# Kernel optimization log

Measured on AMD Instinct MI355X. Metric: run time of the kernel, lower is better.

Reference implementation:

```python
import jax, jax.numpy as jnp
import numpy as np

K = 5
BN_EPS = 1e-5


def _knn(xyz1, xyz2, embedding_lens):
    # squared pairwise distances [B, N, S]
    d2 = (jnp.sum(xyz1 ** 2, -1)[:, :, None]
          + jnp.sum(xyz2 ** 2, -1)[:, None, :]
          - 2.0 * jnp.einsum('bnc,bsc->bns', xyz1, xyz2))
    S = xyz2.shape[1]
    valid2 = jnp.arange(S)[None, :] < embedding_lens[:, None]  # [B, S]
    d2 = jnp.where(valid2[:, None, :], d2, jnp.float32(1e10))
    neg, idx = jax.lax.top_k(-d2, K)  # K smallest distances
    return -neg, idx  # squared dists [B,N,K], indices [B,N,K]


def _masked_bn(x, mask_f, gamma, beta):
    # x: [B, N, C]; mask_f: [B, N, 1] float; stats over valid positions only
    cnt = jnp.sum(mask_f)
    mean = jnp.sum(x * mask_f, axis=(0, 1)) / cnt
    var = jnp.sum(((x - mean) ** 2) * mask_f, axis=(0, 1)) / cnt
    return (x - mean) * jax.lax.rsqrt(var + BN_EPS) * gamma + beta


def setup_inputs() -> dict:
    key = jax.random.key(0)
    ks = jax.random.split(key, 8)
    B, N, S, D1, D2 = 16, 2048, 512, 384, 384
    xyz1 = jax.random.normal(ks[0], (B, N, 3), jnp.float32)
    xyz2 = jax.random.normal(ks[1], (B, S, 3), jnp.float32)
    points1 = jax.random.normal(ks[2], (B, N, D1), jnp.float32)
    points2 = jax.random.normal(ks[3], (B, S, D2), jnp.float32)
    point_lens = jax.random.randint(ks[4], (B,), N // 2, N + 1).astype(jnp.int32)
    embedding_lens = jax.random.randint(ks[5], (B,), S // 2, S + 1).astype(jnp.int32)
    point_mask = jnp.arange(N)[None, :] < point_lens[:, None]  # [B, N] bool
    Cin = D1 + D2
    W0 = jax.random.normal(ks[6], (768, Cin), jnp.float32) * (1.0 / np.sqrt(Cin))
    W1 = jax.random.normal(ks[7], (384, 768), jnp.float32) * (1.0 / np.sqrt(768))
    return dict(xyz1=xyz1, xyz2=xyz2, points1=points1, points2=points2,
                point_lens=point_lens, embedding_lens=embedding_lens,
                point_mask=point_mask,
                W0=W0, g0=jnp.ones((768,), jnp.float32), b0=jnp.zeros((768,), jnp.float32),
                W1=W1, g1=jnp.ones((384,), jnp.float32), b1=jnp.zeros((384,), jnp.float32))


def reference(xyz1, xyz2, points1, points2, point_lens, embedding_lens,
              point_mask, W0, g0, b0, W1, g1, b1):
    B, N, _ = xyz1.shape
    D2 = points2.shape[-1]
    dists, idx = _knn(xyz1[..., :3], xyz2, embedding_lens)
    eps = jnp.finfo(dists.dtype).eps
    dist_recip = 1.0 / (dists + eps)                    # [B, N, K]
    weight = dist_recip / jnp.sum(dist_recip, axis=2, keepdims=True)
    # masked gather: points2[b, idx[b,n,k], :] -> [B, N, K, D2]
    gathered = jnp.take_along_axis(points2, idx.reshape(B, N * K)[..., None],
                                   axis=1).reshape(B, N, K, D2)
    interp = jnp.sum(gathered * weight[..., None], axis=2)  # [B, N, D2]
    x = jnp.concatenate([points1, interp], axis=-1)          # [B, N, D1+D2]
    mask_f = point_mask.astype(x.dtype)[..., None]           # [B, N, 1]
    for W, g, b in ((W0, g0, b0), (W1, g1, b1)):
        x = jnp.einsum('bnc,dc->bnd', x, W)  # 1x1 conv, no bias
        x = jax.nn.relu(_masked_bn(x, mask_f, g, b))
    return x
```

## Files before the change

kernel.cpp:

```cpp
#include <hip/hip_runtime.h>
#include <cstdint>
#include <cstddef>

typedef unsigned short u16;
typedef __bf16 bf16x8 __attribute__((ext_vector_type(8)));
typedef float    f32x4 __attribute__((ext_vector_type(4)));
typedef unsigned int u32x4 __attribute__((ext_vector_type(4)));
typedef unsigned short u16x4 __attribute__((ext_vector_type(4)));

constexpr int BB   = 16;
constexpr int NN   = 2048;
constexpr int SS   = 512;
constexpr int DD   = 384;
constexpr int CIN  = 768;
constexpr int HID  = 768;
constexpr int OUTC = 384;
constexpr int MROWS = BB * NN;
constexpr float KNN_EPS = 1.1920929e-07f;
constexpr float BN_EPS  = 1e-5f;

constexpr size_t OFF_W0B  = 0;
constexpr size_t OFF_W1B  = OFF_W0B  + (size_t)HID*CIN*2;
constexpr size_t OFF_IDX  = OFF_W1B  + (size_t)OUTC*HID*2;
constexpr size_t OFF_WGT  = OFF_IDX  + (size_t)MROWS*5*4;
constexpr size_t OFF_SUM1 = OFF_WGT  + (size_t)MROWS*5*4;
constexpr size_t OFF_SUM2 = OFF_SUM1 + (size_t)HID*2*4;
constexpr size_t OFF_COEF1= OFF_SUM2 + (size_t)OUTC*2*4;
constexpr size_t OFF_COEF2= OFF_COEF1+ (size_t)HID*2*4;
constexpr size_t OFF_XCAT = OFF_COEF2+ (size_t)OUTC*2*4;
constexpr size_t OFF_H1   = OFF_XCAT + (size_t)MROWS*CIN*2;

__device__ inline float bf2f(u16 u){ unsigned int i = ((unsigned int)u)<<16; float f; __builtin_memcpy(&f,&i,4); return f; }
__device__ inline u16 f2bf(float f){ unsigned int x; __builtin_memcpy(&x,&f,4);
  unsigned int r = (x + 0x7fffu + ((x>>16)&1u)) >> 16; return (u16)r; }

__device__ inline void async16(const void* g, void* l){
  __builtin_amdgcn_global_load_lds((const __attribute__((address_space(1))) void*)g,
                                   (__attribute__((address_space(3))) void*)l, 16, 0, 0);
}

__global__ void cvtw_kernel(const float* __restrict__ W0, const float* __restrict__ W1,
                            u16* __restrict__ W0b, u16* __restrict__ W1b){
  int t = blockIdx.x*256 + threadIdx.x;
  if (t < HID*CIN)  W0b[t] = f2bf(W0[t]);
  if (t < OUTC*HID) W1b[t] = f2bf(W1[t]);
}

__global__ __launch_bounds__(256) void knn_kernel(const float* __restrict__ xyz1,
                                                  const float* __restrict__ xyz2,
                                                  const int* __restrict__ elens,
                                                  int* __restrict__ idxO, float* __restrict__ wO){
  __shared__ f32x4 sp[SS];
  const int tid = threadIdx.x;
  const int wv = tid >> 6, lane = tid & 63;
  const int wg = blockIdx.x*4 + wv;
  const int b = wg >> 11;
  const int n = wg & (NN-1);
  for (int s = tid; s < SS; s += 256){
    float x = xyz2[((size_t)b*SS + s)*3 + 0];
    float y = xyz2[((size_t)b*SS + s)*3 + 1];
    float z = xyz2[((size_t)b*SS + s)*3 + 2];
    f32x4 v; v[0]=x; v[1]=y; v[2]=z; v[3]=x*x+y*y+z*z;
    sp[s]=v;
  }
  __syncthreads();
  const size_t qoff = ((size_t)b*NN + n)*3;
  const float qx = xyz1[qoff+0], qy = xyz1[qoff+1], qz = xyz1[qoff+2];
  const float qq = qx*qx + qy*qy + qz*qz;
  const int Sl = elens[b];

  float d0=1e30f,d1=1e30f,d2v=1e30f,d3=1e30f,d4=1e30f;
  int   i0=0,i1=0,i2=0,i3=0,i4=0;
  #pragma unroll
  for (int j=0;j<8;j++){
    const int s = lane + j*64;
    f32x4 v = sp[s];
    float d = (s < Sl) ? (qq + v[3] - 2.f*(qx*v[0] + qy*v[1] + qz*v[2])) : 1e30f;
    bool lt4=d<d4, lt3=d<d3, lt2=d<d2v, lt1=d<d1, lt0=d<d0;
    float nd4 = lt3 ? d3 : (lt4 ? d : d4); int ni4 = lt3 ? i3 : (lt4 ? s : i4);
    float nd3 = lt2 ? d2v: (lt3 ? d : d3); int ni3 = lt2 ? i2 : (lt3 ? s : i3);
    float nd2 = lt1 ? d1 : (lt2 ? d : d2v);int ni2 = lt1 ? i1 : (lt2 ? s : i2);
    float nd1 = lt0 ? d0 : (lt1 ? d : d1); int ni1 = lt0 ? i0 : (lt1 ? s : i1);
    float nd0 = lt0 ? d  : d0;             int ni0 = lt0 ? s  : i0;
    d4=nd4;i4=ni4; d3=nd3;i3=ni3; d2v=nd2;i2=ni2; d1=nd1;i1=ni1; d0=nd0;i0=ni0;
  }
  float outd[5]; int outi[5];
  #pragma unroll
  for (int r=0;r<5;r++){
    float bd = d0; int bs = i0;
    #pragma unroll
    for (int m=1;m<64;m<<=1){
      float od = __shfl_xor(bd, m, 64);
      int   os = __shfl_xor(bs, m, 64);
      if (od < bd || (od == bd && os < bs)){ bd = od; bs = os; }
    }
    outd[r]=bd; outi[r]=bs;
    if (d0 == bd && i0 == bs){ d0=d1;i0=i1; d1=d2v;i1=i2; d2v=d3;i2=i3; d3=d4;i3=i4; d4=1e30f;i4=0; }
  }
  if (lane == 0){
    float r0=1.f/(outd[0]+KNN_EPS), r1=1.f/(outd[1]+KNN_EPS), r2=1.f/(outd[2]+KNN_EPS),
          r3=1.f/(outd[3]+KNN_EPS), r4=1.f/(outd[4]+KNN_EPS);
    float inv = 1.f/(r0+r1+r2+r3+r4);
    size_t base = (size_t)wg*5;
    idxO[base+0]=outi[0]; idxO[base+1]=outi[1]; idxO[base+2]=outi[2]; idxO[base+3]=outi[3]; idxO[base+4]=outi[4];
    wO[base+0]=r0*inv; wO[base+1]=r1*inv; wO[base+2]=r2*inv; wO[base+3]=r3*inv; wO[base+4]=r4*inv;
  }
}

__global__ __launch_bounds__(384) void xcat_kernel(const float* __restrict__ p1,
                                                   const float* __restrict__ p2,
                                                   const int* __restrict__ idx,
                                                   const float* __restrict__ wgt,
                                                   u16* __restrict__ xcat){
  const int t = threadIdx.x;
  const int rloc = t / 96, c4 = t % 96;
  const int row = blockIdx.x*4 + rloc;
  const int b = row >> 11;
  const int c = c4*4;
  f32x4 v1 = *reinterpret_cast<const f32x4*>(p1 + (size_t)row*DD + c);
  size_t ib = (size_t)row*5;
  f32x4 acc = {0.f,0.f,0.f,0.f};
  #pragma unroll
  for (int k=0;k<5;k++){
    int id = idx[ib+k]; float w = wgt[ib+k];
    f32x4 g = *reinterpret_cast<const f32x4*>(p2 + ((size_t)b*SS + id)*DD + c);
    #pragma unroll
    for (int j=0;j<4;j++) acc[j] += w * g[j];
  }
  u16x4 o1, o2;
  #pragma unroll
  for (int j=0;j<4;j++){ o1[j] = f2bf(v1[j]); o2[j] = f2bf(acc[j]); }
  *reinterpret_cast<u16x4*>(xcat + (size_t)row*CIN + c)      = o1;
  *reinterpret_cast<u16x4*>(xcat + (size_t)row*CIN + DD + c) = o2;
}

__global__ __launch_bounds__(512, 6) void gemm1_kernel(const u16* __restrict__ A,
                                                       const u16* __restrict__ Bw,
                                                       u16* __restrict__ Cout,
                                                       const int* __restrict__ plen,
                                                       float* __restrict__ sums){
  constexpr int K   = CIN;
  constexpr int NC  = HID;
  constexpr int GX  = NC/128;
  constexpr int NT  = K/32;
  constexpr int NWG = GX*256;
  constexpr int CPX = NWG/8;
  __shared__ u16 Ash[2][128*32];
  __shared__ u16 Bsh[2][128*32];
  const int tid  = threadIdx.x;
  const int lane = tid & 63, wv = tid >> 6;
  const int wr = wv >> 2, wc = wv & 3;
  const int l15 = lane & 15, l16 = lane >> 4;
  const int swz = (l15 >> 1) & 3;

  const int logical = (blockIdx.x & 7)*CPX + (blockIdx.x >> 3);
  const int bn = logical % GX, bm = logical / GX;

  const int srow = tid >> 2;
  const int sk4  = (tid & 3) ^ ((tid >> 3) & 3);
  const u16* gA = A  + (size_t)(bm*128 + srow)*K + sk4*8;
  const u16* gB = Bw + (size_t)(bn*128 + srow)*K + sk4*8;
  const int dst = (wv*64)*16;

  auto stageA = [&](int tt, int bi){ async16(gA + tt*32, (char*)&Ash[bi][0] + dst); };
  auto stageB = [&](int tt, int bi){ async16(gB + tt*32, (char*)&Bsh[bi][0] + dst); };

  int aoff[4], boff[2];
  #pragma unroll
  for (int m=0;m<4;m++) aoff[m] = (wr*64 + m*16 + l15)*32 + ((l16 ^ swz) << 3);
  #pragma unroll
  for (int n=0;n<2;n++) boff[n] = (wc*32 + n*16 + l15)*32 + ((l16 ^ swz) << 3);

  f32x4 acc[4][2] = {};

  stageA(0,0); stageB(0,0); stageA(1,1); stageB(1,1);
  asm volatile("s_waitcnt vmcnt(2)" ::: "memory");
  __builtin_amdgcn_s_barrier();
  __builtin_amdgcn_sched_barrier(0);

  for (int t=0; t<NT; ++t){
    const int cur = t & 1;
    const int tt = (t+2 < NT) ? (t+2) : (NT-1);
    bf16x8 af0 = *reinterpret_cast<const bf16x8*>(&Ash[cur][aoff[0]]);
    bf16x8 af1 = *reinterpret_cast<const bf16x8*>(&Ash[cur][aoff[1]]);
    bf16x8 af2 = *reinterpret_cast<const bf16x8*>(&Ash[cur][aoff[2]]);
    bf16x8 af3 = *reinterpret_cast<const bf16x8*>(&Ash[cur][aoff[3]]);
    bf16x8 bv0 = *reinterpret_cast<const bf16x8*>(&Bsh[cur][boff[0]]);
    asm volatile("s_waitcnt lgkmcnt(0)" ::: "memory");
    __builtin_amdgcn_s_barrier();
    __builtin_amdgcn_sched_barrier(0);
    stageA(tt, cur);
    __builtin_amdgcn_s_setprio(1);
    acc[0][0] = __builtin_amdgcn_mfma_f32_16x16x32_bf16(af0, bv0, acc[0][0], 0,0,0);
    acc[1][0] = __builtin_amdgcn_mfma_f32_16x16x32_bf16(af1, bv0, acc[1][0], 0,0,0);
    acc[2][0] = __builtin_amdgcn_mfma_f32_16x16x32_bf16(af2, bv0, acc[2][0], 0,0,0);
    acc[3][0] = __builtin_amdgcn_mfma_f32_16x16x32_bf16(af3, bv0, acc[3][0], 0,0,0);
    __builtin_amdgcn_s_setprio(0);
    bf16x8 bv1 = *reinterpret_cast<const bf16x8*>(&Bsh[cur][boff[1]]);
    asm volatile("s_waitcnt lgkmcnt(0)" ::: "memory");
    __builtin_amdgcn_s_barrier();
    __builtin_amdgcn_sched_barrier(0);
    stageB(tt, cur);
    __builtin_amdgcn_s_setprio(1);
    acc[0][1] = __builtin_amdgcn_mfma_f32_16x16x32_bf16(af0, bv1, acc[0][1], 0,0,0);
    acc[1][1] = __builtin_amdgcn_mfma_f32_16x16x32_bf16(af1, bv1, acc[1][1], 0,0,0);
    acc[2][1] = __builtin_amdgcn_mfma_f32_16x16x32_bf16(af2, bv1, acc[2][1], 0,0,0);
    acc[3][1] = __builtin_amdgcn_mfma_f32_16x16x32_bf16(af3, bv1, acc[3][1], 0,0,0);
    __builtin_amdgcn_s_setprio(0);
    asm volatile("s_waitcnt vmcnt(2)" ::: "memory");
    __builtin_amdgcn_s_barrier();
    __builtin_amdgcn_sched_barrier(0);
  }
  asm volatile("s_waitcnt vmcnt(0)" ::: "memory");
  __syncthreads();

  #pragma unroll
  for (int m=0;m<4;m++){
    int r0 = bm*128 + wr*64 + m*16 + l16*4;
    #pragma unroll
    for (int n=0;n<2;n++){
      int c = bn*128 + wc*32 + n*16 + l15;
      #pragma unroll
      for (int r=0;r<4;r++)
        Cout[(size_t)(r0+r)*NC + c] = f2bf(acc[m][n][r]);
    }
  }

  const int pl = plen[bm >> 4];
  const int rbase = (bm & 15)*128 + wr*64 + l16*4;
  float cs[2] = {0.f,0.f}, cs2[2] = {0.f,0.f};
  #pragma unroll
  for (int m=0;m<4;m++){
    #pragma unroll
    for (int r=0;r<4;r++){
      if (rbase + m*16 + r < pl){
        #pragma unroll
        for (int n=0;n<2;n++){
          float v = acc[m][n][r];
          cs[n] += v; cs2[n] += v*v;
        }
      }
    }
  }
  #pragma unroll
  for (int n=0;n<2;n++){
    cs[n]  += __shfl_xor(cs[n], 16, 64);  cs[n]  += __shfl_xor(cs[n], 32, 64);
    cs2[n] += __shfl_xor(cs2[n], 16, 64); cs2[n] += __shfl_xor(cs2[n], 32, 64);
  }
  float* lsum = (float*)&Ash[0][0];
  if (tid < 256) lsum[tid] = 0.f;
  __syncthreads();
  if (l16 == 0){
    #pragma unroll
    for (int n=0;n<2;n++){
      int col = wc*32 + n*16 + l15;
      atomicAdd(&lsum[col], cs[n]);
      atomicAdd(&lsum[128 + col], cs2[n]);
    }
  }
  __syncthreads();
  if (tid < 128)       atomicAdd(&sums[bn*128 + tid], lsum[tid]);
  else if (tid < 256)  atomicAdd(&sums[NC + bn*128 + (tid-128)], lsum[tid]);
}

__global__ void coef_kernel(const float* __restrict__ sums, const int* __restrict__ plen,
                            const float* __restrict__ g, const float* __restrict__ bta,
                            float* __restrict__ coef, int C){
  int c = threadIdx.x;
  if (c >= C) return;
  float cnt = 0.f;
  for (int b=0;b<BB;b++) cnt += (float)plen[b];
  float mean = sums[c] / cnt;
  float var  = sums[C + c] / cnt - mean*mean;
  var = fmaxf(var, 0.f);
  float a = g[c] * rsqrtf(var + BN_EPS);
  coef[c] = a;
  coef[C + c] = bta[c] - mean*a;
}

__global__ __launch_bounds__(256) void gemm2_kernel(const u16* __restrict__ A,
                                                    const u16* __restrict__ Bw,
                                                    float* __restrict__ Cout,
                                                    const int* __restrict__ plen,
                                                    float* __restrict__ sums,
                                                    const float* __restrict__ cf){
  constexpr int GX = 3;
  constexpr int K  = HID;
  constexpr int NC = GX*128;
  constexpr int NSTEP = K/32;
  constexpr int NWG = GX*256;
  constexpr int CPX = NWG/8;
  __shared__ u16 As[2][128*32];
  __shared__ u16 Bs[3][128*32];
  const int tid  = threadIdx.x;
  const int lane = tid & 63, wv = tid >> 6;
  const int wr = wv >> 1, wc = wv & 1;
  const int l15 = lane & 15, l16 = lane >> 4;
  const int sw  = (l15 >> 1) & 3;

  const int logical = (blockIdx.x & 7)*CPX + (blockIdx.x >> 3);
  const int bn = logical % GX, bm = logical / GX;

  int c8S[2], ldso[2];
  const u16* Ab[2]; const u16* Bb[2];
  #pragma unroll
  for (int j=0;j<2;j++){
    int ch = j*256 + wv*64 + lane;
    int row = ch >> 2;
    int c8 = (ch & 3) ^ ((ch >> 3) & 3);
    c8S[j] = c8;
    ldso[j] = (j*256 + wv*64)*16;
    Ab[j] = A  + (size_t)(bm*128 + row)*K + c8*8;
    Bb[j] = Bw + (size_t)(bn*128 + row)*K + c8*8;
  }

  auto stageB = [&](int nb, int kt){
    #pragma unroll
    for (int j=0;j<2;j++) async16(Bb[j] + kt*32, (char*)&Bs[nb][0] + ldso[j]);
  };
  u32x4 hv0, hv1;
  auto loadA = [&](int kt){
    hv0 = *reinterpret_cast<const u32x4*>(Ab[0] + kt*32);
    hv1 = *reinterpret_cast<const u32x4*>(Ab[1] + kt*32);
  };
  auto bnwrite = [&](int nb, int kt){
    #pragma unroll
    for (int j=0;j<2;j++){
      const int k0 = kt*32 + c8S[j]*8;
      float av[8], bv[8];
      *reinterpret_cast<f32x4*>(av)   = *reinterpret_cast<const f32x4*>(cf + k0);
      *reinterpret_cast<f32x4*>(av+4) = *reinterpret_cast<const f32x4*>(cf + k0 + 4);
      *reinterpret_cast<f32x4*>(bv)   = *reinterpret_cast<const f32x4*>(cf + K + k0);
      *reinterpret_cast<f32x4*>(bv+4) = *reinterpret_cast<const f32x4*>(cf + K + k0 + 4);
      u32x4 v = j ? hv1 : hv0; u32x4 o;
      #pragma unroll
      for (int q=0;q<4;q++){
        float lo = bf2f((u16)(v[q] & 0xffffu));
        float hi = bf2f((u16)(v[q] >> 16));
        lo = fmaxf(lo*av[2*q]   + bv[2*q],   0.f);
        hi = fmaxf(hi*av[2*q+1] + bv[2*q+1], 0.f);
        o[q] = (unsigned int)f2bf(lo) | ((unsigned int)f2bf(hi) << 16);
      }
      *reinterpret_cast<u32x4*>((char*)&As[nb][0] + ldso[j] + lane*16) = o;
    }
  };

  f32x4 acc[4][4] = {};

  loadA(0);
  __builtin_amdgcn_sched_barrier(0);
  stageB(0, 0); stageB(1, 1);
  bnwrite(0, 0);
  asm volatile("s_waitcnt vmcnt(2) lgkmcnt(0)" ::: "memory");
  __builtin_amdgcn_s_barrier();

  int rb = 0, wb = 2;
  for (int kt=0; kt<NSTEP; ++kt){
    const bool pf1 = (kt+1 < NSTEP), pf2 = (kt+2 < NSTEP);
    if (pf1) loadA(kt+1);
    __builtin_amdgcn_sched_barrier(0);
    if (pf2) stageB(wb, kt+2);

    bf16x8 af[4], bfr[4];
    const int aslot = kt & 1;
    #pragma unroll
    for (int m=0;m<4;m++){
      int r = wr*64 + m*16 + l15;
      af[m] = *reinterpret_cast<const bf16x8*>(&As[aslot][r*32 + ((l16 ^ sw) << 3)]);
    }
    #pragma unroll
    for (int n=0;n<4;n++){
      int c = wc*64 + n*16 + l15;
      bfr[n] = *reinterpret_cast<const bf16x8*>(&Bs[rb][c*32 + ((l16 ^ sw) << 3)]);
    }
    #pragma unroll
    for (int m=0;m<4;m++)
      #pragma unroll
      for (int n=0;n<4;n++)
        acc[m][n] = __builtin_amdgcn_mfma_f32_16x16x32_bf16(af[m], bfr[n], acc[m][n], 0, 0, 0);

    if (pf1) bnwrite((kt+1)&1, kt+1);

    if (pf1){
      if (pf2) asm volatile("s_waitcnt vmcnt(2) lgkmcnt(0)" ::: "memory");
      else     asm volatile("s_waitcnt vmcnt(0) lgkmcnt(0)" ::: "memory");
      __builtin_amdgcn_s_barrier();
    }
    rb = (rb==2) ? 0 : rb+1;
    wb = (wb==2) ? 0 : wb+1;
  }

  #pragma unroll
  for (int m=0;m<4;m++){
    int r0 = bm*128 + wr*64 + m*16 + l16*4;
    #pragma unroll
    for (int n=0;n<4;n++){
      int c = bn*128 + wc*64 + n*16 + l15;
      #pragma unroll
      for (int r=0;r<4;r++)
        Cout[(size_t)(r0+r)*NC + c] = acc[m][n][r];
    }
  }

  const int pl = plen[bm >> 4];
  const int rbase = (bm & 15)*128 + wr*64 + l16*4;
  float cs[4] = {0.f,0.f,0.f,0.f}, cs2[4] = {0.f,0.f,0.f,0.f};
  #pragma unroll
  for (int m=0;m<4;m++){
    #pragma unroll
    for (int r=0;r<4;r++){
      if (rbase + m*16 + r < pl){
        #pragma unroll
        for (int n=0;n<4;n++){
          float v = acc[m][n][r];
          cs[n] += v; cs2[n] += v*v;
        }
      }
    }
  }
  #pragma unroll
  for (int n=0;n<4;n++){
    cs[n]  += __shfl_xor(cs[n], 16, 64);  cs[n]  += __shfl_xor(cs[n], 32, 64);
    cs2[n] += __shfl_xor(cs2[n], 16, 64); cs2[n] += __shfl_xor(cs2[n], 32, 64);
  }
  float* lsum = (float*)&As[0][0];
  lsum[tid] = 0.f;
  __syncthreads();
  if (l16 == 0){
    #pragma unroll
    for (int n=0;n<4;n++){
      int col = wc*64 + n*16 + l15;
      atomicAdd(&lsum[col], cs[n]);
      atomicAdd(&lsum[128 + col], cs2[n]);
    }
  }
  __syncthreads();
  if (tid < 128)       atomicAdd(&sums[bn*128 + tid], lsum[tid]);
  else                 atomicAdd(&sums[NC + bn*128 + (tid-128)], lsum[tid]);
}

__global__ __launch_bounds__(256) void final_kernel(float* __restrict__ Y,
                                                    const float* __restrict__ coef){
  size_t t = (size_t)blockIdx.x*256 + threadIdx.x;
  size_t f = t*4;
  int c = (int)(f % (size_t)OUTC);
  f32x4 v = *reinterpret_cast<const f32x4*>(Y + f);
  #pragma unroll
  for (int j=0;j<4;j++)
    v[j] = fmaxf(v[j]*coef[c+j] + coef[OUTC+c+j], 0.f);
  *reinterpret_cast<f32x4*>(Y + f) = v;
}

extern "C" void kernel_launch(void* const* d_in, const int* in_sizes, int n_in,
                              void* d_out, int out_size, void* d_ws, size_t ws_size,
                              hipStream_t stream){
  (void)in_sizes; (void)n_in; (void)out_size; (void)ws_size;
  const float* xyz1 = (const float*)d_in[0];
  const float* xyz2 = (const float*)d_in[1];
  const float* p1   = (const float*)d_in[2];
  const float* p2   = (const float*)d_in[3];
  const int*   plen = (const int*)d_in[4];
  const int*   elen = (const int*)d_in[5];
  const float* W0   = (const float*)d_in[7];
  const float* g0   = (const float*)d_in[8];
  const float* b0   = (const float*)d_in[9];
  const float* W1   = (const float*)d_in[10];
  const float* g1   = (const float*)d_in[11];
  const float* b1   = (const float*)d_in[12];
  float* out = (float*)d_out;
  char*  ws  = (char*)d_ws;

  u16*   W0b  = (u16*)  (ws + OFF_W0B);
  u16*   W1b  = (u16*)  (ws + OFF_W1B);
  int*   idxb = (int*)  (ws + OFF_IDX);
  float* wgtb = (float*)(ws + OFF_WGT);
  float* sum1 = (float*)(ws + OFF_SUM1);
  float* sum2 = (float*)(ws + OFF_SUM2);
  float* coef1= (float*)(ws + OFF_COEF1);
  float* coef2= (float*)(ws + OFF_COEF2);
  u16*   xcat = (u16*)  (ws + OFF_XCAT);
  u16*   h1   = (u16*)  (ws + OFF_H1);

  hipMemsetAsync(ws + OFF_SUM1, 0, (size_t)(HID*2 + OUTC*2)*4, stream);

  cvtw_kernel<<<(HID*CIN + 255)/256, 256, 0, stream>>>(W0, W1, W0b, W1b);
  knn_kernel<<<MROWS/4, 256, 0, stream>>>(xyz1, xyz2, elen, idxb, wgtb);
  xcat_kernel<<<MROWS/4, 384, 0, stream>>>(p1, p2, idxb, wgtb, xcat);

  gemm1_kernel<<<6*256, 512, 0, stream>>>(xcat, W0b, h1, plen, sum1);
  coef_kernel<<<1, HID, 0, stream>>>(sum1, plen, g0, b0, coef1, HID);

  gemm2_kernel<<<3*256, 256, 0, stream>>>(h1, W1b, out, plen, sum2, coef1);
  coef_kernel<<<1, OUTC, 0, stream>>>(sum2, plen, g1, b1, coef2, OUTC);
  final_kernel<<<(size_t)MROWS*OUTC/4/256, 256, 0, stream>>>(out, coef2);
}
```

Before: 187.4 us.

## Fold BN coef kernels into consumers, store gemm2 output as bf16, pre-convert points2

Removes both coef kernels and the memset: BN coefficients are computed per block inside gemm2 and final_kernel, and the sum zeroing moves into the conversion kernel. gemm2 writes its pre-BN output as bf16 into the reused xcat buffer, and final_kernel reads it and writes fp32 output, which cuts intermediate write/read traffic. When the workspace is large enough, points2 is converted to bf16 so the gather loads half the bytes. The cost is extra rounding of the pre-BN activations and of points2, redundant coefficient computation in every block, and a larger conversion launch.

```diff
diff --git a/kernel.cpp b/kernel.cpp
--- a/kernel.cpp
+++ b/kernel.cpp
@@ -25,10 +25,10 @@
 constexpr size_t OFF_WGT  = OFF_IDX  + (size_t)MROWS*5*4;
 constexpr size_t OFF_SUM1 = OFF_WGT  + (size_t)MROWS*5*4;
 constexpr size_t OFF_SUM2 = OFF_SUM1 + (size_t)HID*2*4;
-constexpr size_t OFF_COEF1= OFF_SUM2 + (size_t)OUTC*2*4;
-constexpr size_t OFF_COEF2= OFF_COEF1+ (size_t)HID*2*4;
-constexpr size_t OFF_XCAT = OFF_COEF2+ (size_t)OUTC*2*4;
+constexpr size_t OFF_XCAT = OFF_SUM2 + (size_t)OUTC*2*4;
 constexpr size_t OFF_H1   = OFF_XCAT + (size_t)MROWS*CIN*2;
+constexpr size_t OFF_P2B  = OFF_H1   + (size_t)MROWS*HID*2;
+constexpr size_t NEED_P2B = OFF_P2B  + (size_t)BB*SS*DD*2;
 
 __device__ inline float bf2f(u16 u){ unsigned int i = ((unsigned int)u)<<16; float f; __builtin_memcpy(&f,&i,4); return f; }
 __device__ inline u16 f2bf(float f){ unsigned int x; __builtin_memcpy(&x,&f,4);
@@ -40,10 +40,14 @@
 }
 
 __global__ void cvtw_kernel(const float* __restrict__ W0, const float* __restrict__ W1,
-                            u16* __restrict__ W0b, u16* __restrict__ W1b){
+                            const float* __restrict__ p2,
+                            u16* __restrict__ W0b, u16* __restrict__ W1b,
+                            u16* __restrict__ p2b, float* __restrict__ sums){
   int t = blockIdx.x*256 + threadIdx.x;
   if (t < HID*CIN)  W0b[t] = f2bf(W0[t]);
   if (t < OUTC*HID) W1b[t] = f2bf(W1[t]);
+  if (p2b != nullptr && t < BB*SS*DD) p2b[t] = f2bf(p2[t]);
+  if (t < (HID + OUTC)*2) sums[t] = 0.f;
 }
 
 __global__ __launch_bounds__(256) void knn_kernel(const float* __restrict__ xyz1,
@@ -107,8 +111,10 @@
   }
 }
 
+template<bool BF16G>
 __global__ __launch_bounds__(384) void xcat_kernel(const float* __restrict__ p1,
                                                    const float* __restrict__ p2,
+                                                   const u16* __restrict__ p2b,
                                                    const int* __restrict__ idx,
                                                    const float* __restrict__ wgt,
                                                    u16* __restrict__ xcat){
@@ -123,9 +129,15 @@
   #pragma unroll
   for (int k=0;k<5;k++){
     int id = idx[ib+k]; float w = wgt[ib+k];
-    f32x4 g = *reinterpret_cast<const f32x4*>(p2 + ((size_t)b*SS + id)*DD + c);
-    #pragma unroll
-    for (int j=0;j<4;j++) acc[j] += w * g[j];
+    if (BF16G){
+      u16x4 g = *reinterpret_cast<const u16x4*>(p2b + ((size_t)b*SS + id)*DD + c);
+      #pragma unroll
+      for (int j=0;j<4;j++) acc[j] += w * bf2f(g[j]);
+    } else {
+      f32x4 g = *reinterpret_cast<const f32x4*>(p2 + ((size_t)b*SS + id)*DD + c);
+      #pragma unroll
+      for (int j=0;j<4;j++) acc[j] += w * g[j];
+    }
   }
   u16x4 o1, o2;
   #pragma unroll
@@ -263,27 +275,14 @@
   else if (tid < 256)  atomicAdd(&sums[NC + bn*128 + (tid-128)], lsum[tid]);
 }
 
-__global__ void coef_kernel(const float* __restrict__ sums, const int* __restrict__ plen,
-                            const float* __restrict__ g, const float* __restrict__ bta,
-                            float* __restrict__ coef, int C){
-  int c = threadIdx.x;
-  if (c >= C) return;
-  float cnt = 0.f;
-  for (int b=0;b<BB;b++) cnt += (float)plen[b];
-  float mean = sums[c] / cnt;
-  float var  = sums[C + c] / cnt - mean*mean;
-  var = fmaxf(var, 0.f);
-  float a = g[c] * rsqrtf(var + BN_EPS);
-  coef[c] = a;
-  coef[C + c] = bta[c] - mean*a;
-}
-
 __global__ __launch_bounds__(256) void gemm2_kernel(const u16* __restrict__ A,
                                                     const u16* __restrict__ Bw,
-                                                    float* __restrict__ Cout,
+                                                    u16* __restrict__ Yout,
                                                     const int* __restrict__ plen,
                                                     float* __restrict__ sums,
-                                                    const float* __restrict__ cf){
+                                                    const float* __restrict__ sum1,
+                                                    const float* __restrict__ g0,
+                                                    const float* __restrict__ b0){
   constexpr int GX = 3;
   constexpr int K  = HID;
   constexpr int NC = GX*128;
@@ -292,6 +291,7 @@
   constexpr int CPX = NWG/8;
   __shared__ u16 As[2][128*32];
   __shared__ u16 Bs[3][128*32];
+  __shared__ float cfl[HID*2];
   const int tid  = threadIdx.x;
   const int lane = tid & 63, wv = tid >> 6;
   const int wr = wv >> 1, wc = wv & 1;
@@ -328,10 +328,10 @@
     for (int j=0;j<2;j++){
       const int k0 = kt*32 + c8S[j]*8;
       float av[8], bv[8];
-      *reinterpret_cast<f32x4*>(av)   = *reinterpret_cast<const f32x4*>(cf + k0);
-      *reinterpret_cast<f32x4*>(av+4) = *reinterpret_cast<const f32x4*>(cf + k0 + 4);
-      *reinterpret_cast<f32x4*>(bv)   = *reinterpret_cast<const f32x4*>(cf + K + k0);
-      *reinterpret_cast<f32x4*>(bv+4) = *reinterpret_cast<const f32x4*>(cf + K + k0 + 4);
+      *reinterpret_cast<f32x4*>(av)   = *reinterpret_cast<const f32x4*>(cfl + k0);
+      *reinterpret_cast<f32x4*>(av+4) = *reinterpret_cast<const f32x4*>(cfl + k0 + 4);
+      *reinterpret_cast<f32x4*>(bv)   = *reinterpret_cast<const f32x4*>(cfl + K + k0);
+      *reinterpret_cast<f32x4*>(bv+4) = *reinterpret_cast<const f32x4*>(cfl + K + k0 + 4);
       u32x4 v = j ? hv1 : hv0; u32x4 o;
       #pragma unroll
       for (int q=0;q<4;q++){
@@ -350,6 +350,20 @@
   loadA(0);
   __builtin_amdgcn_sched_barrier(0);
   stageB(0, 0); stageB(1, 1);
+  {
+    float cnt = 0.f;
+    #pragma unroll
+    for (int b=0;b<BB;b++) cnt += (float)plen[b];
+    const float icnt = 1.f / cnt;
+    for (int c = tid; c < HID; c += 256){
+      float mean = sum1[c] * icnt;
+      float var  = fmaxf(sum1[HID + c]*icnt - mean*mean, 0.f);
+      float a = g0[c] * rsqrtf(var + BN_EPS);
+      cfl[c] = a;
+      cfl[HID + c] = b0[c] - mean*a;
+    }
+  }
+  __syncthreads();
   bnwrite(0, 0);
   asm volatile("s_waitcnt vmcnt(2) lgkmcnt(0)" ::: "memory");
   __builtin_amdgcn_s_barrier();
@@ -398,7 +412,7 @@
       int c = bn*128 + wc*64 + n*16 + l15;
       #pragma unroll
       for (int r=0;r<4;r++)
-        Cout[(size_t)(r0+r)*NC + c] = acc[m][n][r];
+        Yout[(size_t)(r0+r)*NC + c] = f2bf(acc[m][n][r]);
     }
   }
 
@@ -439,22 +453,52 @@
   else                 atomicAdd(&sums[NC + bn*128 + (tid-128)], lsum[tid]);
 }
 
-__global__ __launch_bounds__(256) void final_kernel(float* __restrict__ Y,
-                                                    const float* __restrict__ coef){
-  size_t t = (size_t)blockIdx.x*256 + threadIdx.x;
-  size_t f = t*4;
-  int c = (int)(f % (size_t)OUTC);
-  f32x4 v = *reinterpret_cast<const f32x4*>(Y + f);
-  #pragma unroll
-  for (int j=0;j<4;j++)
-    v[j] = fmaxf(v[j]*coef[c+j] + coef[OUTC+c+j], 0.f);
-  *reinterpret_cast<f32x4*>(Y + f) = v;
+__global__ __launch_bounds__(256) void final_kernel(const u16* __restrict__ Y,
+                                                    float* __restrict__ O,
+                                                    const float* __restrict__ sums,
+                                                    const int* __restrict__ plen,
+                                                    const float* __restrict__ g1,
+                                                    const float* __restrict__ b1){
+  __shared__ float cfl[OUTC*2];
+  const int tid = threadIdx.x;
+  {
+    float cnt = 0.f;
+    #pragma unroll
+    for (int b=0;b<BB;b++) cnt += (float)plen[b];
+    const float icnt = 1.f / cnt;
+    for (int c = tid; c < OUTC; c += 256){
+      float mean = sums[c] * icnt;
+      float var  = fmaxf(sums[OUTC + c]*icnt - mean*mean, 0.f);
+      float a = g1[c] * rsqrtf(var + BN_EPS);
+      cfl[c] = a;
+      cfl[OUTC + c] = b1[c] - mean*a;
+    }
+  }
+  __syncthreads();
+  const size_t base = (size_t)blockIdx.x * 128 * OUTC;
+  for (int i = tid; i < 128*OUTC/8; i += 256){
+    size_t f = base + (size_t)i*8;
+    int c = (int)(f % (size_t)OUTC);
+    u32x4 v = *reinterpret_cast<const u32x4*>(Y + f);
+    f32x4 o0, o1;
+    #pragma unroll
+    for (int j=0;j<4;j++){
+      float lo = bf2f((u16)(v[j] & 0xffffu));
+      float hi = bf2f((u16)(v[j] >> 16));
+      float r0 = fmaxf(lo*cfl[c+2*j]   + cfl[OUTC+c+2*j],   0.f);
+      float r1 = fmaxf(hi*cfl[c+2*j+1] + cfl[OUTC+c+2*j+1], 0.f);
+      if (j < 2){ o0[2*j] = r0; o0[2*j+1] = r1; }
+      else      { o1[2*(j-2)] = r0; o1[2*(j-2)+1] = r1; }
+    }
+    *reinterpret_cast<f32x4*>(O + f)     = o0;
+    *reinterpret_cast<f32x4*>(O + f + 4) = o1;
+  }
 }
 
 extern "C" void kernel_launch(void* const* d_in, const int* in_sizes, int n_in,
                               void* d_out, int out_size, void* d_ws, size_t ws_size,
                               hipStream_t stream){
-  (void)in_sizes; (void)n_in; (void)out_size; (void)ws_size;
+  (void)in_sizes; (void)n_in; (void)out_size;
   const float* xyz1 = (const float*)d_in[0];
   const float* xyz2 = (const float*)d_in[1];
   const float* p1   = (const float*)d_in[2];
@@ -476,21 +520,22 @@
   float* wgtb = (float*)(ws + OFF_WGT);
   float* sum1 = (float*)(ws + OFF_SUM1);
   float* sum2 = (float*)(ws + OFF_SUM2);
-  float* coef1= (float*)(ws + OFF_COEF1);
-  float* coef2= (float*)(ws + OFF_COEF2);
   u16*   xcat = (u16*)  (ws + OFF_XCAT);
   u16*   h1   = (u16*)  (ws + OFF_H1);
-
-  hipMemsetAsync(ws + OFF_SUM1, 0, (size_t)(HID*2 + OUTC*2)*4, stream);
-
-  cvtw_kernel<<<(HID*CIN + 255)/256, 256, 0, stream>>>(W0, W1, W0b, W1b);
+  const bool hasP2b = (ws_size >= NEED_P2B);
+  u16*   p2b  = hasP2b ? (u16*)(ws + OFF_P2B) : nullptr;
+
+  {
+    int maxT = hasP2b ? (BB*SS*DD) : (HID*CIN);
+    cvtw_kernel<<<(maxT + 255)/256, 256, 0, stream>>>(W0, W1, p2, W0b, W1b, p2b, sum1);
+  }
   knn_kernel<<<MROWS/4, 256, 0, stream>>>(xyz1, xyz2, elen, idxb, wgtb);
-  xcat_kernel<<<MROWS/4, 384, 0, stream>>>(p1, p2, idxb, wgtb, xcat);
+  if (hasP2b) xcat_kernel<true ><<<MROWS/4, 384, 0, stream>>>(p1, p2, p2b, idxb, wgtb, xcat);
+  else        xcat_kernel<false><<<MROWS/4, 384, 0, stream>>>(p1, p2, p2b, idxb, wgtb, xcat);
 
   gemm1_kernel<<<6*256, 512, 0, stream>>>(xcat, W0b, h1, plen, sum1);
-  coef_kernel<<<1, HID, 0, stream>>>(sum1, plen, g0, b0, coef1, HID);
-
-  gemm2_kernel<<<3*256, 256, 0, stream>>>(h1, W1b, out, plen, sum2, coef1);
-  coef_kernel<<<1, OUTC, 0, stream>>>(sum2, plen, g1, b1, coef2, OUTC);
-  final_kernel<<<(size_t)MROWS*OUTC/4/256, 256, 0, stream>>>(out, coef2);
-}
+
+  gemm2_kernel<<<3*256, 256, 0, stream>>>(h1, W1b, xcat , plen, sum2, sum1, g0, b0);
+
+  final_kernel<<<MROWS/128, 256, 0, stream>>>(xcat , out, sum2, plen, g1, b1);
+}
```

Measured after the change: 188.1 us. About the same (+0.4%).
